# Performance work log

Measured on AMD Instinct MI355X. Metric: run time of the kernel, lower is better.

Reference implementation:

```python
import jax, jax.numpy as jnp
import numpy as np

BITS = 4
GROUP = 128
PACK = 32 // BITS  # 8 values per int32
MASK = (1 << BITS) - 1


def _unpack_weight(qweight, K, N):
    # qweight: [K//PACK, N] int32; PACK 4-bit values packed along K in each int32
    shifts = jnp.arange(PACK, dtype=jnp.int32) * BITS  # [PACK]
    w = (qweight[:, None, :] >> shifts[None, :, None]) & MASK  # [K//PACK, PACK, N]
    return w.reshape(K, N)


def _unpack_zeros(qzeros, G, N):
    # qzeros: [G, N//PACK] int32; PACK 4-bit values packed along N in each int32
    shifts = jnp.arange(PACK, dtype=jnp.int32) * BITS  # [PACK]
    z = (qzeros[:, :, None] >> shifts[None, None, :]) & MASK  # [G, N//PACK, PACK]
    return z.reshape(G, N)


def setup_inputs() -> dict:
    key = jax.random.key(0)
    k1, k2, k3, k4 = jax.random.split(key, 4)
    B, S, K, N = 4, 1024, 4096, 11008
    G = K // GROUP
    x = jax.random.normal(k1, (B, S, K), dtype=jnp.float32)
    qweight = jax.random.randint(k2, (K // PACK, N), 0, 2147483647, dtype=jnp.int32)
    qzeros = jax.random.randint(k3, (G, N // PACK), 0, 2147483647, dtype=jnp.int32)
    scales = jax.random.uniform(k4, (G, N), dtype=jnp.float32) * 0.01
    return {"x": x, "qweight": qweight, "qzeros": qzeros, "scales": scales}


def reference(x, qweight, qzeros, scales):
    K = x.shape[-1]
    G, N = scales.shape
    # dequantize: W[k, n] = (q[k, n] - zero[g(k), n]) * scale[g(k), n]
    w_q = _unpack_weight(qweight, K, N).astype(jnp.float32)   # [K, N]
    zeros = _unpack_zeros(qzeros, G, N).astype(jnp.float32)   # [G, N]
    gid = jnp.arange(K) // GROUP                              # [K]
    W = (w_q - zeros[gid]) * scales[gid]                      # [K, N]
    return jnp.einsum('bsk,kn->bsn', x, W)
```

## Files before the change

kernel.cpp:

```cpp
#include <hip/hip_runtime.h>


#define BK 32
#define LDK 40
#define TILE_BYTES 10240

typedef _Float16 v8h __attribute__((ext_vector_type(8)));
typedef _Float16 half2v __attribute__((ext_vector_type(2)));
typedef float v4f __attribute__((ext_vector_type(4)));

__device__ __forceinline__ unsigned pkrtz_u32(float a, float b) {
  return __builtin_bit_cast(unsigned, __builtin_amdgcn_cvt_pkrtz(a, b));
}

__device__ __forceinline__ void load_lds_16B(const void* g, void* l) {
  __builtin_amdgcn_global_load_lds(
      (const __attribute__((address_space(1))) unsigned*)g,
      (__attribute__((address_space(3))) unsigned*)l, 16, 0, 0);
}

__device__ __forceinline__ void bar() { asm volatile("s_barrier" ::: "memory"); }

__global__ __launch_bounds__(512)
void prep_a8(const float* __restrict__ x, unsigned short* __restrict__ fa, int K) {
  const int t = blockIdx.x, mt = blockIdx.y;
  unsigned short* tile = fa + (size_t)(mt * (K / 64) + t) * 16384;
#pragma unroll
  for (int p = 0; p < 4; ++p) {
    const int c = threadIdx.x + p * 512;
    const int h = c >> 10, r = (c >> 3) & 127, s = c & 7;
    const float* src = x + (size_t)(mt * 256 + h * 128 + r) * K + t * 64 + s * 8;
    const float4 v0 = ((const float4*)src)[0];
    const float4 v1 = ((const float4*)src)[1];
    uint4 o;
    o.x = pkrtz_u32(v0.x, v0.y); o.y = pkrtz_u32(v0.z, v0.w);
    o.z = pkrtz_u32(v1.x, v1.y); o.w = pkrtz_u32(v1.z, v1.w);
    *(uint4*)(tile + h * 8192 + r * 64 + ((s ^ (r & 7)) << 3)) = o;
  }
}

__global__ __launch_bounds__(512)
void prep_b8(const unsigned* __restrict__ qweight,
             const unsigned* __restrict__ qzeros,
             const float* __restrict__ scales,
             unsigned short* __restrict__ fb, int N, int K) {
  const int nt = blockIdx.x, t = blockIdx.y;
  const int g = t >> 1;
  unsigned short* tile = fb + (size_t)(nt * (K / 64) + t) * 16384;
#pragma unroll
  for (int p = 0; p < 4; ++p) {
    const int c = threadIdx.x + p * 512;
    const int h = c >> 10, r = (c >> 3) & 127, s = c & 7;
    const int n = nt * 256 + h * 128 + r;
    const unsigned zp = qzeros[(size_t)g * (N >> 3) + (n >> 3)];
    const float sc = scales[(size_t)g * N + n];
    const unsigned z = (zp >> ((n & 7) * 4)) & 15u;
    const unsigned hz_u = 0x64006400u | z | (z << 16);
    const half2v hz2 = __builtin_bit_cast(half2v, hz_u);
    const half2v hs2 = __builtin_bit_cast(half2v, pkrtz_u32(sc, sc));
    const unsigned qv = qweight[(size_t)(t * 8 + s) * N + n];
    uint4 o;
    unsigned* wp = (unsigned*)&o;
#pragma unroll
    for (int b = 0; b < 4; ++b) {
      const unsigned byte = qv >> (8 * b);
      const unsigned pq = 0x64006400u | (byte & 0xFu) | ((byte & 0xF0u) << 12);
      const half2v w2 = (__builtin_bit_cast(half2v, pq) - hz2) * hs2;
      wp[b] = __builtin_bit_cast(unsigned, w2);
    }
    *(uint4*)(tile + h * 8192 + r * 64 + ((s ^ (r & 7)) << 3)) = o;
  }
}


#define READA4(PA, MB)                                                         \
  _Pragma("unroll") for (int i = 0; i < 4; ++i) {                              \
    aF[i][0] = *(const v8h*)((PA) + ((MB + i) * 16 + lr16) * 128 + koff0);     \
    aF[i][1] = *(const v8h*)((PA) + ((MB + i) * 16 + lr16) * 128 + koff1);     \
  }

#define READB2(PB, BF, NB)                                                     \
  _Pragma("unroll") for (int j = 0; j < 2; ++j) {                              \
    BF[j][0] = *(const v8h*)((PB) + ((NB + j) * 16 + lr16) * 128 + koff0);     \
    BF[j][1] = *(const v8h*)((PB) + ((NB + j) * 16 + lr16) * 128 + koff1);     \
  }

#define MMAQ(MB, NB, BF)                                                       \
  __builtin_amdgcn_s_setprio(1);                                              \
  _Pragma("unroll") for (int i = 0; i < 4; ++i)                                \
  _Pragma("unroll") for (int j = 0; j < 2; ++j) {                              \
    acc[MB + i][NB + j] = __builtin_amdgcn_mfma_f32_16x16x32_f16(              \
        aF[i][0], BF[j][0], acc[MB + i][NB + j], 0, 0, 0);                     \
    acc[MB + i][NB + j] = __builtin_amdgcn_mfma_f32_16x16x32_f16(              \
        aF[i][1], BF[j][1], acc[MB + i][NB + j], 0, 0, 0);                     \
  }                                                                            \
  __builtin_amdgcn_s_setprio(0);

__global__ __launch_bounds__(512, 2)
void qgemm8(const unsigned short* __restrict__ fa,
            const unsigned short* __restrict__ fb,
            float* __restrict__ out, int M, int N, int K) {
  __shared__ __align__(16) short As[2][2][128][64];
  __shared__ __align__(16) short Bs[2][2][128][64];

  const int tid = threadIdx.x;
  const int lane = tid & 63;
  const int wid = tid >> 6;
  const int wr = wid >> 2, wc = wid & 3;
  const int lr16 = lane & 15, hi4 = lane >> 4, l7 = lane & 7;
  const int koff0 = ((hi4 ^ l7) << 4);
  const int koff1 = (((4 + hi4) ^ l7) << 4);

  const int nmt = M / 256;
  const int nwg = nmt * (N / 256);
  int bid = blockIdx.x;
  {
    const int xcd = bid & 7, idx = bid >> 3;
    const int q = nwg >> 3, r = nwg & 7;
    bid = (xcd < r ? xcd * (q + 1) : r * (q + 1) + (xcd - r) * q) + idx;
  }
  const int mt = bid % nmt;
  const int nt = bid / nmt;

  const int NT = K / 64;
  const int NI = NT / 2;

  const char* srcA = (const char*)fa + (size_t)mt * NT * 32768 + wid * 1024 + lane * 16;
  const char* srcB = (const char*)fb + (size_t)nt * NT * 32768 + wid * 1024 + lane * 16;
  char* ldsA = (char*)&As[0][0][0][0];
  char* ldsB = (char*)&Bs[0][0][0][0];
  char* dstA = ldsA + wid * 1024;
  char* dstB = ldsB + wid * 1024;

  auto stageA = [&](int T, int h) {
    const char* s = srcA + (size_t)T * 32768 + h * 16384;
    char* d = dstA + (T & 1) * 32768 + h * 16384;
    load_lds_16B(s, d);
    load_lds_16B(s + 8192, d + 8192);
  };
  auto stageB = [&](int T, int h) {
    const char* s = srcB + (size_t)T * 32768 + h * 16384;
    char* d = dstB + (T & 1) * 32768 + h * 16384;
    load_lds_16B(s, d);
    load_lds_16B(s + 8192, d + 8192);
  };

  const char* pA[2] = {ldsA + wr * 16384, ldsA + 32768 + wr * 16384};
  const char* pB[2] = {ldsB + (wc >> 1) * 16384 + (wc & 1) * 8192,
                       ldsB + 32768 + (wc >> 1) * 16384 + (wc & 1) * 8192};

  v4f acc[8][4] = {};
  v8h aF[4][2], bL[2][2], bH[2][2];

  stageB(0, 0); stageB(0, 1); stageA(0, 0); stageA(0, 1);
  stageB(1, 0); stageB(1, 1);
  asm volatile("s_waitcnt vmcnt(4)");
  bar();

  for (int it = 0; it < NI; ++it) {
    const int t0 = 2 * it, t1 = 2 * it + 1;
    const bool pf = (it < NI - 1);

    READA4(pA[0], 0);
    READB2(pA[0] == nullptr ? pB[0] : pB[0], bL, 0);
    stageA(t1, 0);
    bar();
    MMAQ(0, 0, bL);
    bar();
    READB2(pB[0], bH, 2);
    stageA(t1, 1);
    bar();
    MMAQ(0, 2, bH);
    bar();
    READA4(pA[0], 4);
    if (pf) stageB(t0 + 2, 0);
    bar();
    MMAQ(4, 0, bL);
    bar();
    if (pf) { stageB(t0 + 2, 1); asm volatile("s_waitcnt vmcnt(4)"); }
    else    { asm volatile("s_waitcnt vmcnt(0)"); }
    bar();
    MMAQ(4, 2, bH);
    bar();

    READA4(pA[1], 0);
    READB2(pB[1], bL, 0);
    if (pf) stageA(t0 + 2, 0);
    bar();
    MMAQ(0, 0, bL);
    bar();
    READB2(pB[1], bH, 2);
    if (pf) stageA(t0 + 2, 1);
    bar();
    MMAQ(0, 2, bH);
    bar();
    READA4(pA[1], 4);
    if (pf) stageB(t1 + 2, 0);
    bar();
    MMAQ(4, 0, bL);
    bar();
    if (pf) { stageB(t1 + 2, 1); asm volatile("s_waitcnt vmcnt(4)"); }
    else    { asm volatile("s_waitcnt vmcnt(0)"); }
    bar();
    MMAQ(4, 2, bH);
    bar();
  }

  const int m0 = mt * 256 + wr * 128;
  const int n0 = nt * 256 + wc * 64;
#pragma unroll
  for (int mi = 0; mi < 8; ++mi) {
#pragma unroll
    for (int ni = 0; ni < 4; ++ni) {
#pragma unroll
      for (int r = 0; r < 4; ++r) {
        const int row = m0 + mi * 16 + hi4 * 4 + r;
        const int col = n0 + ni * 16 + lr16;
        out[(size_t)row * N + col] = acc[mi][ni][r];
      }
    }
  }
}

__global__ __launch_bounds__(320)
void prep_x(const float* __restrict__ x, unsigned short* __restrict__ xt, int K) {
  const int kt = blockIdx.x, mt = blockIdx.y;
  unsigned short* tile = xt + (size_t)(mt * (K / 32) + kt) * (TILE_BYTES / 2);
#pragma unroll
  for (int p = 0; p < 2; ++p) {
    const int c = threadIdx.x + p * 320;
    const int r = c / 5, j = c - r * 5;
    uint4 o = {0u, 0u, 0u, 0u};
    if (j < 4) {
      const float* src = x + (size_t)(mt * 128 + r) * K + kt * 32 + j * 8;
      const float4 v0 = ((const float4*)src)[0];
      const float4 v1 = ((const float4*)src)[1];
      o.x = pkrtz_u32(v0.x, v0.y); o.y = pkrtz_u32(v0.z, v0.w);
      o.z = pkrtz_u32(v1.x, v1.y); o.w = pkrtz_u32(v1.z, v1.w);
    }
    *(uint4*)((char*)tile + (size_t)c * 16) = o;
  }
}

__global__ __launch_bounds__(512, 4)
void qgemm_dma(const unsigned short* __restrict__ xt,
               const unsigned* __restrict__ qweight,
               const unsigned* __restrict__ qzeros,
               const float* __restrict__ scales,
               float* __restrict__ out, int M, int N, int K) {
  __shared__ __align__(16) short As[128][LDK];
  __shared__ __align__(16) short Bs[256][LDK];

  const int tid = threadIdx.x;
  const int lane = tid & 63;
  const int wid = tid >> 6;
  const int n0 = blockIdx.x * 256;
  const int m0 = blockIdx.y * 128;
  const int mt = blockIdx.y;
  const int wm = (wid >> 2) * 64;
  const int wn = (wid & 3) * 64;
  const int lr = lane & 15;
  const int lk = (lane >> 4) * 8;

  const int b_n = tid & 255;
  const int b_kr0 = tid >> 8;
  const int gn = n0 + b_n;
  const unsigned* qwb = qweight + (size_t)b_kr0 * N + gn;

  const char* xt_b = (const char*)xt;
  const int NT = K / BK;

  v4f acc[4][4] = {};

  unsigned b0c, b1c, zpc;
  float scc;
  auto load_b = [&](int t, unsigned& b0, unsigned& b1, unsigned& zp, float& sc) {
    const int kk = t * BK;
    const size_t qoff = (size_t)(kk >> 3) * N;
    b0 = qwb[qoff];
    b1 = qwb[qoff + 2 * (size_t)N];
    const int g = kk >> 7;
    zp = qzeros[(size_t)g * (N >> 3) + (gn >> 3)];
    sc = scales[(size_t)g * N + gn];
  };
  load_b(0, b0c, b1c, zpc, scc);

#pragma unroll 2
  for (int t = 0; t < NT; ++t) {
    {
      const char* g = xt_b + (size_t)(mt * NT + t) * TILE_BYTES +
                      (size_t)wid * 1024 + (size_t)lane * 16;
      char* l = ((char*)&As[0][0]) + wid * 1024;
      load_lds_16B(g, l);
      if (wid < 2) load_lds_16B(g + 8 * 1024, l + 8 * 1024);
    }
    {
      const unsigned z = (zpc >> ((gn & 7) * 4)) & 15u;
      const unsigned hz_u = 0x64006400u | z | (z << 16);
      const half2v hz2 = __builtin_bit_cast(half2v, hz_u);
      const half2v hs2 = __builtin_bit_cast(half2v, pkrtz_u32(scc, scc));
      const unsigned qvs[2] = {b0c, b1c};
#pragma unroll
      for (int q = 0; q < 2; ++q) {
        const int kr = b_kr0 + q * 2;
        const unsigned qv = qvs[q];
        uint4 wv;
        unsigned* wp = (unsigned*)&wv;
#pragma unroll
        for (int j = 0; j < 4; ++j) {
          const unsigned byte = qv >> (8 * j);
          const unsigned pq = 0x64006400u | (byte & 0xFu) | ((byte & 0xF0u) << 12);
          const half2v w2 = (__builtin_bit_cast(half2v, pq) - hz2) * hs2;
          wp[j] = __builtin_bit_cast(unsigned, w2);
        }
        *(uint4*)(&Bs[b_n][kr * 8]) = wv;
      }
    }

    __syncthreads();

    unsigned b0n, b1n, zpn;
    float scn;
    const int tn = (t + 1 < NT) ? (t + 1) : t;
    load_b(tn, b0n, b1n, zpn, scn);

    v8h af[4], bfr[4];
#pragma unroll
    for (int i = 0; i < 4; ++i) {
      af[i] = *(const v8h*)(&As[wm + i * 16 + lr][lk]);
      bfr[i] = *(const v8h*)(&Bs[wn + i * 16 + lr][lk]);
    }
#pragma unroll
    for (int mi = 0; mi < 4; ++mi) {
#pragma unroll
      for (int ni = 0; ni < 4; ++ni) {
        acc[mi][ni] = __builtin_amdgcn_mfma_f32_16x16x32_f16(
            af[mi], bfr[ni], acc[mi][ni], 0, 0, 0);
      }
    }

    __syncthreads();

    b0c = b0n; b1c = b1n; zpc = zpn; scc = scn;
  }

#pragma unroll
  for (int mi = 0; mi < 4; ++mi) {
#pragma unroll
    for (int ni = 0; ni < 4; ++ni) {
#pragma unroll
      for (int r = 0; r < 4; ++r) {
        const int row = m0 + wm + mi * 16 + (lane >> 4) * 4 + r;
        const int col = n0 + wn + ni * 16 + lr;
        out[(size_t)row * N + col] = acc[mi][ni][r];
      }
    }
  }
}

__global__ __launch_bounds__(256, 2)
void qgemm_fused(const float* __restrict__ x,
                 const unsigned* __restrict__ qweight,
                 const unsigned* __restrict__ qzeros,
                 const float* __restrict__ scales,
                 float* __restrict__ out, int M, int N, int K) {
  __shared__ short As[128][LDK];
  __shared__ short Bs[128][LDK];

  const int tid = threadIdx.x;
  const int lane = tid & 63;
  const int wid = tid >> 6;
  const int n0 = blockIdx.x * 128;
  const int m0 = blockIdx.y * 128;
  const int wm = (wid >> 1) * 64;
  const int wn = (wid & 1) * 64;
  const int lr = lane & 15;
  const int lk = (lane >> 4) * 8;

  const int a_row = tid >> 3;
  const int a_col = (tid & 7) * 4;
  const int b_n = tid & 127;
  const int b_kr0 = tid >> 7;
  const int gn = n0 + b_n;

  const float* xb = x + (size_t)(m0 + a_row) * K + a_col;
  const unsigned* qwb = qweight + (size_t)b_kr0 * N + gn;

  v4f acc[4][4] = {};
  const int NT = K / BK;

  float4 axc[4];
  unsigned b0c, b1c, zpc;
  float scc;

  auto load_step = [&](int t, float4 ax[4], unsigned& b0, unsigned& b1,
                       unsigned& zp, float& sc) {
    const int kk = t * BK;
#pragma unroll
    for (int p = 0; p < 4; ++p)
      ax[p] = *(const float4*)(xb + (size_t)(p * 32) * K + kk);
    const size_t qoff = (size_t)(kk >> 3) * N;
    b0 = qwb[qoff];
    b1 = qwb[qoff + 2 * (size_t)N];
    const int g = kk >> 7;
    zp = qzeros[(size_t)g * (N >> 3) + (gn >> 3)];
    sc = scales[(size_t)g * N + gn];
  };

  load_step(0, axc, b0c, b1c, zpc, scc);

#pragma unroll 2
  for (int t = 0; t < NT; ++t) {
    const unsigned z = (zpc >> ((gn & 7) * 4)) & 15u;
    const unsigned hz_u = 0x64006400u | z | (z << 16);
    const half2v hz2 = __builtin_bit_cast(half2v, hz_u);
    const half2v hs2 = __builtin_bit_cast(half2v, pkrtz_u32(scc, scc));

#pragma unroll
    for (int p = 0; p < 4; ++p) {
      const int row = p * 32 + a_row;
      uint2 pv;
      pv.x = pkrtz_u32(axc[p].x, axc[p].y);
      pv.y = pkrtz_u32(axc[p].z, axc[p].w);
      *(uint2*)(&As[row][a_col]) = pv;
    }
    {
      const unsigned qvs[2] = {b0c, b1c};
#pragma unroll
      for (int q = 0; q < 2; ++q) {
        const int kr = b_kr0 + q * 2;
        const unsigned qv = qvs[q];
        uint4 wv;
        unsigned* wp = (unsigned*)&wv;
#pragma unroll
        for (int j = 0; j < 4; ++j) {
          const unsigned byte = qv >> (8 * j);
          const unsigned pq = 0x64006400u | (byte & 0xFu) | ((byte & 0xF0u) << 12);
          const half2v w2 = (__builtin_bit_cast(half2v, pq) - hz2) * hs2;
          wp[j] = __builtin_bit_cast(unsigned, w2);
        }
        *(uint4*)(&Bs[b_n][kr * 8]) = wv;
      }
    }

    __syncthreads();

    float4 axn[4];
    unsigned b0n, b1n, zpn;
    float scn;
    const int tn = (t + 1 < NT) ? (t + 1) : t;
    load_step(tn, axn, b0n, b1n, zpn, scn);

    v8h af[4], bfr[4];
#pragma unroll
    for (int i = 0; i < 4; ++i) {
      af[i] = *(const v8h*)(&As[wm + i * 16 + lr][lk]);
      bfr[i] = *(const v8h*)(&Bs[wn + i * 16 + lr][lk]);
    }
#pragma unroll
    for (int mi = 0; mi < 4; ++mi) {
#pragma unroll
      for (int ni = 0; ni < 4; ++ni) {
        acc[mi][ni] = __builtin_amdgcn_mfma_f32_16x16x32_f16(
            af[mi], bfr[ni], acc[mi][ni], 0, 0, 0);
      }
    }

    __syncthreads();

#pragma unroll
    for (int p = 0; p < 4; ++p) axc[p] = axn[p];
    b0c = b0n; b1c = b1n; zpc = zpn; scc = scn;
  }

#pragma unroll
  for (int mi = 0; mi < 4; ++mi) {
#pragma unroll
    for (int ni = 0; ni < 4; ++ni) {
#pragma unroll
      for (int r = 0; r < 4; ++r) {
        const int row = m0 + wm + mi * 16 + (lane >> 4) * 4 + r;
        const int col = n0 + wn + ni * 16 + lr;
        out[(size_t)row * N + col] = acc[mi][ni][r];
      }
    }
  }
}

extern "C" void kernel_launch(void* const* d_in, const int* in_sizes, int n_in,
                              void* d_out, int out_size, void* d_ws, size_t ws_size,
                              hipStream_t stream) {
  const float* x = (const float*)d_in[0];
  const unsigned* qweight = (const unsigned*)d_in[1];
  const unsigned* qzeros = (const unsigned*)d_in[2];
  const float* scales = (const float*)d_in[3];
  float* out = (float*)d_out;

  const int K = 4096;
  const int N = 11008;
  const int M = in_sizes[0] / K;

  const size_t A8 = (size_t)(M / 256) * (K / 64) * 32768;
  const size_t B8 = (size_t)(N / 256) * (K / 64) * 32768;
  const size_t A_BYTES = (size_t)(M / 128) * (K / 32) * TILE_BYTES;

  if ((M % 256 == 0) && ws_size >= A8 + B8) {
    unsigned short* fa = (unsigned short*)d_ws;
    unsigned short* fb = (unsigned short*)((char*)d_ws + A8);
    prep_a8<<<dim3(K / 64, M / 256), 512, 0, stream>>>(x, fa, K);
    prep_b8<<<dim3(N / 256, K / 64), 512, 0, stream>>>(qweight, qzeros, scales, fb, N, K);
    qgemm8<<<dim3((M / 256) * (N / 256)), 512, 0, stream>>>(fa, fb, out, M, N, K);
  } else if (ws_size >= A_BYTES) {
    unsigned short* xt = (unsigned short*)d_ws;
    prep_x<<<dim3(K / 32, M / 128), 320, 0, stream>>>(x, xt, K);
    qgemm_dma<<<dim3(N / 256, M / 128), 512, 0, stream>>>(xt, qweight, qzeros, scales,
                                                          out, M, N, K);
  } else {
    qgemm_fused<<<dim3(N / 128, M / 128), 256, 0, stream>>>(x, qweight, qzeros, scales,
                                                            out, M, N, K);
  }
}
```

Measured before the change: 622.1 us.

## Merge prep kernels into one launch and drop redundant GEMM barriers

Fuses the activation-conversion and weight-dequantization prep kernels into a single launch that splits work by block index, removing one kernel launch and the gap between the two. Inside the main GEMM loop, about half the s_barrier calls are removed and the two B-stage prefetches are grouped together before the wait, so waves stall less often on workgroup synchronization. Dropping barriers risks LDS read/write hazards if a stage overwrites a buffer that other waves are still reading.

```diff
diff --git a/kernel.cpp b/kernel.cpp
--- a/kernel.cpp
+++ b/kernel.cpp
@@ -22,53 +22,58 @@
 __device__ __forceinline__ void bar() { asm volatile("s_barrier" ::: "memory"); }
 
 __global__ __launch_bounds__(512)
-void prep_a8(const float* __restrict__ x, unsigned short* __restrict__ fa, int K) {
-  const int t = blockIdx.x, mt = blockIdx.y;
-  unsigned short* tile = fa + (size_t)(mt * (K / 64) + t) * 16384;
-#pragma unroll
-  for (int p = 0; p < 4; ++p) {
-    const int c = threadIdx.x + p * 512;
-    const int h = c >> 10, r = (c >> 3) & 127, s = c & 7;
-    const float* src = x + (size_t)(mt * 256 + h * 128 + r) * K + t * 64 + s * 8;
-    const float4 v0 = ((const float4*)src)[0];
-    const float4 v1 = ((const float4*)src)[1];
-    uint4 o;
-    o.x = pkrtz_u32(v0.x, v0.y); o.y = pkrtz_u32(v0.z, v0.w);
-    o.z = pkrtz_u32(v1.x, v1.y); o.w = pkrtz_u32(v1.z, v1.w);
-    *(uint4*)(tile + h * 8192 + r * 64 + ((s ^ (r & 7)) << 3)) = o;
-  }
-}
-
-__global__ __launch_bounds__(512)
-void prep_b8(const unsigned* __restrict__ qweight,
+void prep_ab(const float* __restrict__ x,
+             const unsigned* __restrict__ qweight,
              const unsigned* __restrict__ qzeros,
              const float* __restrict__ scales,
-             unsigned short* __restrict__ fb, int N, int K) {
-  const int nt = blockIdx.x, t = blockIdx.y;
-  const int g = t >> 1;
-  unsigned short* tile = fb + (size_t)(nt * (K / 64) + t) * 16384;
-#pragma unroll
-  for (int p = 0; p < 4; ++p) {
-    const int c = threadIdx.x + p * 512;
-    const int h = c >> 10, r = (c >> 3) & 127, s = c & 7;
-    const int n = nt * 256 + h * 128 + r;
-    const unsigned zp = qzeros[(size_t)g * (N >> 3) + (n >> 3)];
-    const float sc = scales[(size_t)g * N + n];
-    const unsigned z = (zp >> ((n & 7) * 4)) & 15u;
-    const unsigned hz_u = 0x64006400u | z | (z << 16);
-    const half2v hz2 = __builtin_bit_cast(half2v, hz_u);
-    const half2v hs2 = __builtin_bit_cast(half2v, pkrtz_u32(sc, sc));
-    const unsigned qv = qweight[(size_t)(t * 8 + s) * N + n];
-    uint4 o;
-    unsigned* wp = (unsigned*)&o;
-#pragma unroll
-    for (int b = 0; b < 4; ++b) {
-      const unsigned byte = qv >> (8 * b);
-      const unsigned pq = 0x64006400u | (byte & 0xFu) | ((byte & 0xF0u) << 12);
-      const half2v w2 = (__builtin_bit_cast(half2v, pq) - hz2) * hs2;
-      wp[b] = __builtin_bit_cast(unsigned, w2);
-    }
-    *(uint4*)(tile + h * 8192 + r * 64 + ((s ^ (r & 7)) << 3)) = o;
+             unsigned short* __restrict__ fa,
+             unsigned short* __restrict__ fb, int M, int N, int K) {
+  const int KT = K / 64;
+  const int NA = (M / 256) * KT;
+  int b = blockIdx.x;
+  if (b < NA) {
+    const int mt = b / KT, t = b - mt * KT;
+    unsigned short* tile = fa + (size_t)(mt * KT + t) * 16384;
+#pragma unroll
+    for (int p = 0; p < 4; ++p) {
+      const int c = threadIdx.x + p * 512;
+      const int h = c >> 10, r = (c >> 3) & 127, s = c & 7;
+      const float* src = x + (size_t)(mt * 256 + h * 128 + r) * K + t * 64 + s * 8;
+      const float4 v0 = ((const float4*)src)[0];
+      const float4 v1 = ((const float4*)src)[1];
+      uint4 o;
+      o.x = pkrtz_u32(v0.x, v0.y); o.y = pkrtz_u32(v0.z, v0.w);
+      o.z = pkrtz_u32(v1.x, v1.y); o.w = pkrtz_u32(v1.z, v1.w);
+      *(uint4*)(tile + h * 8192 + r * 64 + ((s ^ (r & 7)) << 3)) = o;
+    }
+  } else {
+    b -= NA;
+    const int nt = b / KT, t = b - nt * KT;
+    const int g = t >> 1;
+    unsigned short* tile = fb + (size_t)(nt * KT + t) * 16384;
+#pragma unroll
+    for (int p = 0; p < 4; ++p) {
+      const int c = threadIdx.x + p * 512;
+      const int h = c >> 10, r = (c >> 3) & 127, s = c & 7;
+      const int n = nt * 256 + h * 128 + r;
+      const unsigned zp = qzeros[(size_t)g * (N >> 3) + (n >> 3)];
+      const float sc = scales[(size_t)g * N + n];
+      const unsigned z = (zp >> ((n & 7) * 4)) & 15u;
+      const unsigned hz_u = 0x64006400u | z | (z << 16);
+      const half2v hz2 = __builtin_bit_cast(half2v, hz_u);
+      const half2v hs2 = __builtin_bit_cast(half2v, pkrtz_u32(sc, sc));
+      const unsigned qv = qweight[(size_t)(t * 8 + s) * N + n];
+      uint4 o;
+      unsigned* wp = (unsigned*)&o;
+#pragma unroll
+      for (int bb = 0; bb < 4; ++bb) {
+        const unsigned byte = qv >> (8 * bb);
+        const unsigned pq = 0x64006400u | (byte & 0xFu) | ((byte & 0xF0u) << 12);
+        const half2v w2 = (__builtin_bit_cast(half2v, pq) - hz2) * hs2;
+        wp[bb] = __builtin_bit_cast(unsigned, w2);
+      }
+      *(uint4*)(tile + h * 8192 + r * 64 + ((s ^ (r & 7)) << 3)) = o;
+    }
   }
 }
 
@@ -162,48 +167,40 @@
     const bool pf = (it < NI - 1);
 
     READA4(pA[0], 0);
-    READB2(pA[0] == nullptr ? pB[0] : pB[0], bL, 0);
+    READB2(pB[0], bL, 0);
     stageA(t1, 0);
     bar();
     MMAQ(0, 0, bL);
-    bar();
     READB2(pB[0], bH, 2);
     stageA(t1, 1);
     bar();
     MMAQ(0, 2, bH);
-    bar();
     READA4(pA[0], 4);
-    if (pf) stageB(t0 + 2, 0);
     bar();
     MMAQ(4, 0, bL);
-    bar();
-    if (pf) { stageB(t0 + 2, 1); asm volatile("s_waitcnt vmcnt(4)"); }
+    if (pf) { stageB(t0 + 2, 0); stageB(t0 + 2, 1);
+              asm volatile("s_waitcnt vmcnt(4)"); }
     else    { asm volatile("s_waitcnt vmcnt(0)"); }
     bar();
     MMAQ(4, 2, bH);
-    bar();
 
     READA4(pA[1], 0);
     READB2(pB[1], bL, 0);
     if (pf) stageA(t0 + 2, 0);
     bar();
     MMAQ(0, 0, bL);
-    bar();
     READB2(pB[1], bH, 2);
     if (pf) stageA(t0 + 2, 1);
     bar();
     MMAQ(0, 2, bH);
-    bar();
     READA4(pA[1], 4);
-    if (pf) stageB(t1 + 2, 0);
     bar();
     MMAQ(4, 0, bL);
-    bar();
-    if (pf) { stageB(t1 + 2, 1); asm volatile("s_waitcnt vmcnt(4)"); }
+    if (pf) { stageB(t1 + 2, 0); stageB(t1 + 2, 1);
+              asm volatile("s_waitcnt vmcnt(4)"); }
     else    { asm volatile("s_waitcnt vmcnt(0)"); }
     bar();
     MMAQ(4, 2, bH);
-    bar();
   }
 
   const int m0 = mt * 256 + wr * 128;
@@ -507,8 +504,8 @@
   if ((M % 256 == 0) && ws_size >= A8 + B8) {
     unsigned short* fa = (unsigned short*)d_ws;
     unsigned short* fb = (unsigned short*)((char*)d_ws + A8);
-    prep_a8<<<dim3(K / 64, M / 256), 512, 0, stream>>>(x, fa, K);
-    prep_b8<<<dim3(N / 256, K / 64), 512, 0, stream>>>(qweight, qzeros, scales, fb, N, K);
+    const int nblk = (M / 256) * (K / 64) + (N / 256) * (K / 64);
+    prep_ab<<<dim3(nblk), 512, 0, stream>>>(x, qweight, qzeros, scales, fa, fb, M, N, K);
     qgemm8<<<dim3((M / 256) * (N / 256)), 512, 0, stream>>>(fa, fb, out, M, N, K);
   } else if (ws_size >= A_BYTES) {
     unsigned short* xt = (unsigned short*)d_ws;
```

Result: faster. 587.3 us (-5.6%).
